# Optimization experiments

Hardware: AMD Instinct MI355X
Metric: run time of the kernel (lower is better)

The kernel has to match this reference:

```python
import jax, jax.numpy as jnp
import numpy as np

B, T, N, D, H = 16, 12, 325, 64, 4
E = 2600
NEG_SLOPE = 0.2
LN_EPS = 1e-5
SM_EPS = 1e-16


def setup_inputs() -> dict:
    key = jax.random.key(0)
    ks = jax.random.split(key, 8)
    x = jax.random.normal(ks[0], (B, T, N, D), dtype=jnp.float32)
    edge_index = jax.random.randint(ks[1], (2, E), 0, N, dtype=jnp.int64)
    W = jax.random.normal(ks[2], (D, H, D), dtype=jnp.float32) * 0.05   # lin weight, [in, heads, out]
    att_src = jax.random.normal(ks[3], (H, D), dtype=jnp.float32) * 0.05
    att_dst = jax.random.normal(ks[4], (H, D), dtype=jnp.float32) * 0.05
    bias = jnp.zeros((D,), dtype=jnp.float32)
    gamma = jnp.ones((D,), dtype=jnp.float32)
    beta = jnp.zeros((D,), dtype=jnp.float32)
    return {"x": x, "W": W, "att_src": att_src, "att_dst": att_dst,
            "bias": bias, "gamma": gamma, "beta": beta, "edge_index": edge_index}


def reference(x, W, att_src, att_dst, bias, gamma, beta, edge_index):
    b, t, n, d = x.shape
    bt = b * t
    xb = x.reshape(bt, n, d)

    # add self-loops (GATConv default add_self_loops=True)
    loops = jnp.arange(n, dtype=edge_index.dtype)
    src = jnp.concatenate([edge_index[0], loops])  # message source j
    dst = jnp.concatenate([edge_index[1], loops])  # message target i

    # per-head linear projection, node axis leading for segment ops: [N, BT, H, D]
    xp = jnp.einsum('bnd,dhf->nbhf', xb, W)

    a_src = jnp.einsum('nbhf,hf->nbh', xp, att_src)  # [N, BT, H]
    a_dst = jnp.einsum('nbhf,hf->nbh', xp, att_dst)

    alpha = a_src[src] + a_dst[dst]                  # [Etot, BT, H]
    alpha = jnp.where(alpha >= 0, alpha, NEG_SLOPE * alpha)

    # segment softmax over incoming edges of each dst node
    m = jax.ops.segment_max(alpha, dst, num_segments=n)        # [N, BT, H]
    e = jnp.exp(alpha - m[dst])
    s = jax.ops.segment_sum(e, dst, num_segments=n)            # [N, BT, H]
    coef = e / (s[dst] + SM_EPS)                               # [Etot, BT, H]

    # weighted scatter-sum aggregation
    msgs = coef[..., None] * xp[src]                           # [Etot, BT, H, D]
    out = jax.ops.segment_sum(msgs, dst, num_segments=n)       # [N, BT, H, D]

    out = out.mean(axis=2) + bias                              # concat=False -> head mean; [N, BT, D]
    out = out.transpose(1, 0, 2).reshape(b, t, n, d)

    # residual + LayerNorm
    y = x + out
    mu = y.mean(axis=-1, keepdims=True)
    var = y.var(axis=-1, keepdims=True)
    return (y - mu) * jax.lax.rsqrt(var + LN_EPS) * gamma + beta
```

## Files before the change

kernel.cpp:

```cpp
#include <hip/hip_runtime.h>

#define Nn 325
#define Dd 64
#define Hh 4
#define Ee 2600
#define BT 192
#define ETOT (Ee+Nn)
#define NROWS (BT*Nn)
#define XPS 136

#define XP_B   (Nn * XPS * 2)
#define COEF_B (ETOT * 8)
#define SMEM_BYTES (XP_B + COEF_B + 2600 + 2600 + ((Nn + 1) * 4) + (ETOT * 4) + (Nn * 4))

typedef __attribute__((ext_vector_type(8))) short bf16x8;
typedef __attribute__((ext_vector_type(4))) float f32x4;

static __device__ __forceinline__ short f2bf(float f) {
    union { float f; unsigned u; } v; v.f = f;
    unsigned r = v.u + 0x7fffu + ((v.u >> 16) & 1u);
    return (short)(r >> 16);
}
static __device__ __forceinline__ float bf_lo(unsigned p) {
    union { unsigned u; float f; } v; v.u = p << 16; return v.f;
}
static __device__ __forceinline__ float bf_hi(unsigned p) {
    union { unsigned u; float f; } v; v.u = p & 0xffff0000u; return v.f;
}

__global__ __launch_bounds__(256) void k_pre(
    const float* __restrict__ W, unsigned short* __restrict__ Wt,
    const int* __restrict__ ei, int* __restrict__ offs, int* __restrict__ elist,
    int* __restrict__ perm, const float* __restrict__ x,
    unsigned short* __restrict__ xbf)
{
    const int t = threadIdx.x;
    if (blockIdx.x < 64) {
        const int f = blockIdx.x * 256 + t;
        const int thr = f >> 6, idx = f & 63;
        const int ct = idx >> 4, kk = (idx >> 3) & 1, j = idx & 7;
        const int w = thr >> 6, lane = thr & 63;
        const int q = lane >> 4, l16 = lane & 15;
        Wt[f] = (unsigned short)f2bf(
            W[(size_t)(kk * 32 + q * 8 + j) * 256 + w * 64 + ct * 16 + l16]);
        return;
    }
    if (blockIdx.x >= 65) {
        const int bx = blockIdx.x - 65;
        #pragma unroll
        for (int k = 0; k < 8; ++k) {
            const int idx = bx * 2048 + k * 256 + t;
            if (idx < (NROWS * Dd) / 4) {
                float4 v = ((const float4*)x)[idx];
                ushort4 o;
                o.x = (unsigned short)f2bf(v.x);
                o.y = (unsigned short)f2bf(v.y);
                o.z = (unsigned short)f2bf(v.z);
                o.w = (unsigned short)f2bf(v.w);
                ((ushort4*)xbf)[idx] = o;
            }
        }
        return;
    }
    __shared__ int cnt[Nn + 1];
    __shared__ int cur[Nn];
    __shared__ int dh[64];
    __shared__ int startS[64];
    const int lane = t & 63;
    for (int i = t; i <= Nn; i += 256) cnt[i] = 0;
    if (t < 64) dh[t] = 0;
    __syncthreads();
    for (int e = t; e < ETOT; e += 256) {
        int d = (e < Ee) ? ei[Ee + e] : (e - Ee);
        atomicAdd(&cnt[d + 1], 1);
    }
    __syncthreads();
    if (t < 64) {
        int run = 0;
        for (int c = 0; c < 6; ++c) {
            int i = c * 64 + lane;
            int v = (i <= Nn) ? cnt[i] : 0;
            #pragma unroll
            for (int off = 1; off < 64; off <<= 1) {
                int u = __shfl_up(v, off);
                if (lane >= off) v += u;
            }
            v += run;
            if (i <= Nn) cnt[i] = v;
            run = __shfl(v, 63);
        }
    }
    __syncthreads();
    for (int i = t; i <= Nn; i += 256) offs[i] = cnt[i];
    for (int i = t; i < Nn; i += 256) cur[i] = cnt[i];
    for (int n = t; n < Nn; n += 256)
        atomicAdd(&dh[min(cnt[n + 1] - cnt[n], 63)], 1);
    __syncthreads();
    if (t < 64) {
        int v = dh[63 - lane];
        int inc = v;
        #pragma unroll
        for (int off = 1; off < 64; off <<= 1) {
            int u = __shfl_up(inc, off);
            if (lane >= off) inc += u;
        }
        startS[63 - lane] = inc - v;
    }
    __syncthreads();
    for (int e = t; e < ETOT; e += 256) {
        int s, d;
        if (e < Ee) { s = ei[e]; d = ei[Ee + e]; }
        else        { s = e - Ee; d = e - Ee; }
        int slot = atomicAdd(&cur[d], 1);
        elist[slot] = s;
    }
    for (int n = t; n < Nn; n += 256) {
        int slot = atomicAdd(&startS[min(cnt[n + 1] - cnt[n], 63)], 1);
        perm[slot] = n;
    }
}

__global__ __launch_bounds__(1024, 4) void k_fused(
    const float* __restrict__ x, const unsigned short* __restrict__ xbf,
    const unsigned short* __restrict__ Wt,
    const float* __restrict__ att_src, const float* __restrict__ att_dst,
    const int* __restrict__ offs, const int* __restrict__ elist,
    const int* __restrict__ perm,
    const float* __restrict__ bias, const float* __restrict__ gamma,
    const float* __restrict__ beta, float* __restrict__ out)
{
    const int bt   = blockIdx.x;
    const int t    = threadIdx.x;
    const int wv   = t >> 6;
    const int lane = t & 63;
    const int q    = lane >> 4;
    const int l16  = lane & 15;
    const int btN  = bt * Nn;

    extern __shared__ char smem[];
    unsigned short* xpS   = (unsigned short*)smem;
    float2*         coefS = (float2*)(smem + XP_B);
    float*          asrcS = (float*)(smem + XP_B + COEF_B);
    float*          adstS = asrcS + 2 * Nn;
    int*            offsS = (int*)(adstS + 2 * Nn);
    int*            elistS= offsS + (Nn + 1);
    int*            permS = elistS + ETOT;

    for (int i = t; i < ETOT; i += 1024) elistS[i] = elist[i];
    for (int i = t; i <= Nn; i += 1024) offsS[i] = offs[i];
    for (int i = t; i < Nn; i += 1024) permS[i] = perm[i];

    float accO[6][4];
    #pragma unroll
    for (int i = 0; i < 6; ++i)
        accO[i][0] = accO[i][1] = accO[i][2] = accO[i][3] = 0.f;

    const int hh  = wv >> 3;
    const int rtb = wv & 7;
    const int g   = wv * 4 + q;

    #pragma unroll 2
    for (int p = 0; p < 2; ++p) {
        const int h = p * 2 + hh;
        bf16x8 bfr[4][2];
        const bf16x8* wtp = (const bf16x8*)(Wt + (size_t)(h * 64 + lane) * 64);
        #pragma unroll
        for (int ct = 0; ct < 4; ++ct) {
            bfr[ct][0] = wtp[ct * 2];
            bfr[ct][1] = wtp[ct * 2 + 1];
        }
        float avs[4], avd[4];
        #pragma unroll
        for (int ct = 0; ct < 4; ++ct) {
            avs[ct] = att_src[h * 64 + ct * 16 + l16];
            avd[ct] = att_dst[h * 64 + ct * 16 + l16];
        }
        if (p) __syncthreads();

        #pragma unroll
        for (int k3 = 0; k3 < 3; ++k3) {
            const int rt = rtb + 8 * k3;
            if (rt > 20) break;
            const int na = min(rt * 16 + l16, Nn - 1);
            bf16x8 afr[2];
            #pragma unroll
            for (int kk = 0; kk < 2; ++kk)
                afr[kk] = *(const bf16x8*)(xbf + (size_t)(btN + na) * 64 + kk * 32 + q * 8);
            f32x4 acc[4];
            #pragma unroll
            for (int ct = 0; ct < 4; ++ct) {
                acc[ct] = (f32x4){0.f, 0.f, 0.f, 0.f};
                acc[ct] = __builtin_amdgcn_mfma_f32_16x16x32_bf16(afr[0], bfr[ct][0], acc[ct], 0, 0, 0);
                acc[ct] = __builtin_amdgcn_mfma_f32_16x16x32_bf16(afr[1], bfr[ct][1], acc[ct], 0, 0, 0);
            }
            #pragma unroll
            for (int r = 0; r < 4; ++r) {
                const int n = rt * 16 + q * 4 + r;
                float ps = 0.f, pd = 0.f;
                #pragma unroll
                for (int ct = 0; ct < 4; ++ct) {
                    ps = fmaf(acc[ct][r], avs[ct], ps);
                    pd = fmaf(acc[ct][r], avd[ct], pd);
                }
                #pragma unroll
                for (int off = 1; off <= 8; off <<= 1) {
                    ps += __shfl_xor(ps, off);
                    pd += __shfl_xor(pd, off);
                }
                if (l16 == 0 && n < Nn) {
                    asrcS[n * 2 + hh] = ps;
                    adstS[n * 2 + hh] = pd;
                }
                if (n < Nn) {
                    #pragma unroll
                    for (int ct = 0; ct < 4; ++ct)
                        xpS[n * XPS + (ct * 16 + l16) * 2 + hh] =
                            (unsigned short)f2bf(acc[ct][r]);
                }
            }
        }
        __syncthreads();

        #pragma unroll
        for (int it = 0; it < 6; ++it) {
            const int rk = it * 64 + g;
            if (rk >= Nn) continue;
            const int n = permS[rk];
            const int o0 = offsS[n];
            int deg = offsS[n + 1] - o0;
            deg = min(deg, 48);
            const float adn0 = adstS[n * 2], adn1 = adstS[n * 2 + 1];
            float ex0[3], ex1[3];
            float m0 = -3e38f, m1 = -3e38f;
            #pragma unroll
            for (int r = 0; r < 3; ++r) {
                float a0 = -3e38f, a1 = -3e38f;
                if (r * 16 < deg) {
                    const int e = r * 16 + l16;
                    if (e < deg) {
                        const int j = elistS[o0 + e];
                        const float2 as = *(const float2*)(asrcS + j * 2);
                        a0 = as.x + adn0; a1 = as.y + adn1;
                    }
                }
                a0 = (a0 >= 0.f) ? a0 : 0.2f * a0;
                a1 = (a1 >= 0.f) ? a1 : 0.2f * a1;
                ex0[r] = a0; ex1[r] = a1;
                m0 = fmaxf(m0, a0); m1 = fmaxf(m1, a1);
            }
            #pragma unroll
            for (int off = 1; off <= 8; off <<= 1) {
                m0 = fmaxf(m0, __shfl_xor(m0, off));
                m1 = fmaxf(m1, __shfl_xor(m1, off));
            }
            float s0 = 0.f, s1 = 0.f;
            #pragma unroll
            for (int r = 0; r < 3; ++r) if (r * 16 < deg) {
                ex0[r] = __expf(ex0[r] - m0); s0 += ex0[r];
                ex1[r] = __expf(ex1[r] - m1); s1 += ex1[r];
            }
            #pragma unroll
            for (int off = 1; off <= 8; off <<= 1) {
                s0 += __shfl_xor(s0, off);
                s1 += __shfl_xor(s1, off);
            }
            const float i0 = 1.f / (s0 + 1e-16f);
            const float i1 = 1.f / (s1 + 1e-16f);
            #pragma unroll
            for (int r = 0; r < 3; ++r) if (r * 16 < deg) {
                const int e = r * 16 + l16;
                if (e < deg) coefS[o0 + e] = make_float2(ex0[r] * i0, ex1[r] * i1);
            }

            float f0 = 0.f, f1 = 0.f, f2v = 0.f, f3 = 0.f;
            int e2 = 0;
            for (; e2 + 4 <= deg; e2 += 4) {
                const int j0 = elistS[o0 + e2],     j1 = elistS[o0 + e2 + 1];
                const int j2 = elistS[o0 + e2 + 2], j3 = elistS[o0 + e2 + 3];
                const float2 c0 = coefS[o0 + e2],     c1 = coefS[o0 + e2 + 1];
                const float2 c2 = coefS[o0 + e2 + 2], c3 = coefS[o0 + e2 + 3];
                const uint4 r0 = *(const uint4*)((const char*)xpS + j0 * (XPS * 2) + l16 * 16);
                const uint4 r1 = *(const uint4*)((const char*)xpS + j1 * (XPS * 2) + l16 * 16);
                const uint4 r2 = *(const uint4*)((const char*)xpS + j2 * (XPS * 2) + l16 * 16);
                const uint4 r3 = *(const uint4*)((const char*)xpS + j3 * (XPS * 2) + l16 * 16);
                f0  = fmaf(c0.x, bf_lo(r0.x), f0);  f0  = fmaf(c0.y, bf_hi(r0.x), f0);
                f1  = fmaf(c0.x, bf_lo(r0.y), f1);  f1  = fmaf(c0.y, bf_hi(r0.y), f1);
                f2v = fmaf(c0.x, bf_lo(r0.z), f2v); f2v = fmaf(c0.y, bf_hi(r0.z), f2v);
                f3  = fmaf(c0.x, bf_lo(r0.w), f3);  f3  = fmaf(c0.y, bf_hi(r0.w), f3);
                f0  = fmaf(c1.x, bf_lo(r1.x), f0);  f0  = fmaf(c1.y, bf_hi(r1.x), f0);
                f1  = fmaf(c1.x, bf_lo(r1.y), f1);  f1  = fmaf(c1.y, bf_hi(r1.y), f1);
                f2v = fmaf(c1.x, bf_lo(r1.z), f2v); f2v = fmaf(c1.y, bf_hi(r1.z), f2v);
                f3  = fmaf(c1.x, bf_lo(r1.w), f3);  f3  = fmaf(c1.y, bf_hi(r1.w), f3);
                f0  = fmaf(c2.x, bf_lo(r2.x), f0);  f0  = fmaf(c2.y, bf_hi(r2.x), f0);
                f1  = fmaf(c2.x, bf_lo(r2.y), f1);  f1  = fmaf(c2.y, bf_hi(r2.y), f1);
                f2v = fmaf(c2.x, bf_lo(r2.z), f2v); f2v = fmaf(c2.y, bf_hi(r2.z), f2v);
                f3  = fmaf(c2.x, bf_lo(r2.w), f3);  f3  = fmaf(c2.y, bf_hi(r2.w), f3);
                f0  = fmaf(c3.x, bf_lo(r3.x), f0);  f0  = fmaf(c3.y, bf_hi(r3.x), f0);
                f1  = fmaf(c3.x, bf_lo(r3.y), f1);  f1  = fmaf(c3.y, bf_hi(r3.y), f1);
                f2v = fmaf(c3.x, bf_lo(r3.z), f2v); f2v = fmaf(c3.y, bf_hi(r3.z), f2v);
                f3  = fmaf(c3.x, bf_lo(r3.w), f3);  f3  = fmaf(c3.y, bf_hi(r3.w), f3);
            }
            for (; e2 < deg; ++e2) {
                const int ja = elistS[o0 + e2];
                const float2 ca = coefS[o0 + e2];
                const uint4 ra = *(const uint4*)((const char*)xpS + ja * (XPS * 2) + l16 * 16);
                f0  = fmaf(ca.x, bf_lo(ra.x), f0);  f0  = fmaf(ca.y, bf_hi(ra.x), f0);
                f1  = fmaf(ca.x, bf_lo(ra.y), f1);  f1  = fmaf(ca.y, bf_hi(ra.y), f1);
                f2v = fmaf(ca.x, bf_lo(ra.z), f2v); f2v = fmaf(ca.y, bf_hi(ra.z), f2v);
                f3  = fmaf(ca.x, bf_lo(ra.w), f3);  f3  = fmaf(ca.y, bf_hi(ra.w), f3);
            }
            accO[it][0] += f0; accO[it][1] += f1;
            accO[it][2] += f2v; accO[it][3] += f3;
        }
    }

    const int f4 = l16 * 4;
    const float4 ga = *(const float4*)(gamma + f4);
    const float4 be = *(const float4*)(beta + f4);
    const float4 bi = *(const float4*)(bias + f4);
    #pragma unroll
    for (int it = 0; it < 6; ++it) {
        const int rk = it * 64 + g;
        if (rk >= Nn) continue;
        const int n = permS[rk];
        const float4 xv = *(const float4*)(x + (size_t)(btN + n) * 64 + f4);
        const float y0 = xv.x + accO[it][0] * 0.25f + bi.x;
        const float y1 = xv.y + accO[it][1] * 0.25f + bi.y;
        const float y2 = xv.z + accO[it][2] * 0.25f + bi.z;
        const float y3 = xv.w + accO[it][3] * 0.25f + bi.w;
        float s1 = y0 + y1 + y2 + y3;
        float s2 = y0*y0 + y1*y1 + y2*y2 + y3*y3;
        #pragma unroll
        for (int off = 1; off <= 8; off <<= 1) {
            s1 += __shfl_xor(s1, off);
            s2 += __shfl_xor(s2, off);
        }
        const float mu  = s1 * (1.f / 64.f);
        const float var = s2 * (1.f / 64.f) - mu * mu;
        const float rr  = rsqrtf(var + 1e-5f);
        float4 o;
        o.x = (y0 - mu) * rr * ga.x + be.x;
        o.y = (y1 - mu) * rr * ga.y + be.y;
        o.z = (y2 - mu) * rr * ga.z + be.z;
        o.w = (y3 - mu) * rr * ga.w + be.w;
        *(float4*)(out + (size_t)(btN + n) * 64 + f4) = o;
    }
}

extern "C" void kernel_launch(void* const* d_in, const int* in_sizes, int n_in,
                              void* d_out, int out_size, void* d_ws, size_t ws_size,
                              hipStream_t stream)
{
    const float* x       = (const float*)d_in[0];
    const float* W       = (const float*)d_in[1];
    const float* att_src = (const float*)d_in[2];
    const float* att_dst = (const float*)d_in[3];
    const float* bias    = (const float*)d_in[4];
    const float* gamma   = (const float*)d_in[5];
    const float* beta    = (const float*)d_in[6];
    const int*   ei      = (const int*)d_in[7];

    unsigned short* Wt  = (unsigned short*)d_ws;
    unsigned short* xbf = Wt + 16384;
    int* offs  = (int*)(xbf + (size_t)NROWS * Dd);
    int* elist = offs + (Nn + 1);
    int* perm  = elist + ETOT;
    float* out = (float*)d_out;

    hipFuncSetAttribute((const void*)k_fused,
                        hipFuncAttributeMaxDynamicSharedMemorySize, SMEM_BYTES);

    hipLaunchKernelGGL(k_pre, dim3(65 + 488), dim3(256), 0, stream,
                       W, Wt, ei, offs, elist, perm, x, xbf);
    hipLaunchKernelGGL(k_fused, dim3(BT), dim3(1024), SMEM_BYTES, stream,
                       x, xbf, Wt, att_src, att_dst, offs, elist, perm,
                       bias, gamma, beta, out);
}
```

Before: 134.4 us.

## Fold preprocessing kernel into fused GAT kernel and pipeline aggregation loads

Removes the separate preprocessing kernel. Each block now builds the CSR edge list and degree-sorted permutation in shared memory itself, converts W and x to bf16 on the fly from global fp32, and skips the bf16 copy of x in workspace. This avoids a kernel launch and a full write/read round trip of the x-sized bf16 buffer. In exchange every one of the 192 blocks repeats the CSR build and the W conversion with strided scalar loads. The aggregation loop also gains software prefetching of the next edge indices and coefficients, and uses packed float2 FMAs.

```diff
diff --git a/kernel.cpp b/kernel.cpp
--- a/kernel.cpp
+++ b/kernel.cpp
@@ -6,7 +6,6 @@
 #define Ee 2600
 #define BT 192
 #define ETOT (Ee+Nn)
-#define NROWS (BT*Nn)
 #define XPS 136
 
 #define XP_B   (Nn * XPS * 2)
@@ -15,117 +14,23 @@
 
 typedef __attribute__((ext_vector_type(8))) short bf16x8;
 typedef __attribute__((ext_vector_type(4))) float f32x4;
+typedef __attribute__((ext_vector_type(2))) float f32x2;
 
 static __device__ __forceinline__ short f2bf(float f) {
     union { float f; unsigned u; } v; v.f = f;
     unsigned r = v.u + 0x7fffu + ((v.u >> 16) & 1u);
     return (short)(r >> 16);
 }
-static __device__ __forceinline__ float bf_lo(unsigned p) {
-    union { unsigned u; float f; } v; v.u = p << 16; return v.f;
+static __device__ __forceinline__ f32x2 up2(unsigned u) {
+    union { unsigned u; float f; } lo, hi;
+    lo.u = u << 16; hi.u = u & 0xffff0000u;
+    f32x2 r; r.x = lo.f; r.y = hi.f; return r;
 }
-static __device__ __forceinline__ float bf_hi(unsigned p) {
-    union { unsigned u; float f; } v; v.u = p & 0xffff0000u; return v.f;
-}
-
-__global__ __launch_bounds__(256) void k_pre(
-    const float* __restrict__ W, unsigned short* __restrict__ Wt,
-    const int* __restrict__ ei, int* __restrict__ offs, int* __restrict__ elist,
-    int* __restrict__ perm, const float* __restrict__ x,
-    unsigned short* __restrict__ xbf)
-{
-    const int t = threadIdx.x;
-    if (blockIdx.x < 64) {
-        const int f = blockIdx.x * 256 + t;
-        const int thr = f >> 6, idx = f & 63;
-        const int ct = idx >> 4, kk = (idx >> 3) & 1, j = idx & 7;
-        const int w = thr >> 6, lane = thr & 63;
-        const int q = lane >> 4, l16 = lane & 15;
-        Wt[f] = (unsigned short)f2bf(
-            W[(size_t)(kk * 32 + q * 8 + j) * 256 + w * 64 + ct * 16 + l16]);
-        return;
-    }
-    if (blockIdx.x >= 65) {
-        const int bx = blockIdx.x - 65;
-        #pragma unroll
-        for (int k = 0; k < 8; ++k) {
-            const int idx = bx * 2048 + k * 256 + t;
-            if (idx < (NROWS * Dd) / 4) {
-                float4 v = ((const float4*)x)[idx];
-                ushort4 o;
-                o.x = (unsigned short)f2bf(v.x);
-                o.y = (unsigned short)f2bf(v.y);
-                o.z = (unsigned short)f2bf(v.z);
-                o.w = (unsigned short)f2bf(v.w);
-                ((ushort4*)xbf)[idx] = o;
-            }
-        }
-        return;
-    }
-    __shared__ int cnt[Nn + 1];
-    __shared__ int cur[Nn];
-    __shared__ int dh[64];
-    __shared__ int startS[64];
-    const int lane = t & 63;
-    for (int i = t; i <= Nn; i += 256) cnt[i] = 0;
-    if (t < 64) dh[t] = 0;
-    __syncthreads();
-    for (int e = t; e < ETOT; e += 256) {
-        int d = (e < Ee) ? ei[Ee + e] : (e - Ee);
-        atomicAdd(&cnt[d + 1], 1);
-    }
-    __syncthreads();
-    if (t < 64) {
-        int run = 0;
-        for (int c = 0; c < 6; ++c) {
-            int i = c * 64 + lane;
-            int v = (i <= Nn) ? cnt[i] : 0;
-            #pragma unroll
-            for (int off = 1; off < 64; off <<= 1) {
-                int u = __shfl_up(v, off);
-                if (lane >= off) v += u;
-            }
-            v += run;
-            if (i <= Nn) cnt[i] = v;
-            run = __shfl(v, 63);
-        }
-    }
-    __syncthreads();
-    for (int i = t; i <= Nn; i += 256) offs[i] = cnt[i];
-    for (int i = t; i < Nn; i += 256) cur[i] = cnt[i];
-    for (int n = t; n < Nn; n += 256)
-        atomicAdd(&dh[min(cnt[n + 1] - cnt[n], 63)], 1);
-    __syncthreads();
-    if (t < 64) {
-        int v = dh[63 - lane];
-        int inc = v;
-        #pragma unroll
-        for (int off = 1; off < 64; off <<= 1) {
-            int u = __shfl_up(inc, off);
-            if (lane >= off) inc += u;
-        }
-        startS[63 - lane] = inc - v;
-    }
-    __syncthreads();
-    for (int e = t; e < ETOT; e += 256) {
-        int s, d;
-        if (e < Ee) { s = ei[e]; d = ei[Ee + e]; }
-        else        { s = e - Ee; d = e - Ee; }
-        int slot = atomicAdd(&cur[d], 1);
-        elist[slot] = s;
-    }
-    for (int n = t; n < Nn; n += 256) {
-        int slot = atomicAdd(&startS[min(cnt[n + 1] - cnt[n], 63)], 1);
-        perm[slot] = n;
-    }
-}
-
-__global__ __launch_bounds__(1024, 4) void k_fused(
-    const float* __restrict__ x, const unsigned short* __restrict__ xbf,
-    const unsigned short* __restrict__ Wt,
+
+__global__ __launch_bounds__(1024, 4) void k_gat(
+    const float* __restrict__ x, const float* __restrict__ W,
     const float* __restrict__ att_src, const float* __restrict__ att_dst,
-    const int* __restrict__ offs, const int* __restrict__ elist,
-    const int* __restrict__ perm,
+    const int* __restrict__ ei,
     const float* __restrict__ bias, const float* __restrict__ gamma,
     const float* __restrict__ beta, float* __restrict__ out)
 {
@@ -139,21 +44,75 @@
 
     extern __shared__ char smem[];
     unsigned short* xpS   = (unsigned short*)smem;
-    float2*         coefS = (float2*)(smem + XP_B);
+    f32x2*          coefS = (f32x2*)(smem + XP_B);
     float*          asrcS = (float*)(smem + XP_B + COEF_B);
     float*          adstS = asrcS + 2 * Nn;
     int*            offsS = (int*)(adstS + 2 * Nn);
     int*            elistS= offsS + (Nn + 1);
     int*            permS = elistS + ETOT;
-
-    for (int i = t; i < ETOT; i += 1024) elistS[i] = elist[i];
-    for (int i = t; i <= Nn; i += 1024) offsS[i] = offs[i];
-    for (int i = t; i < Nn; i += 1024) permS[i] = perm[i];
-
-    float accO[6][4];
+    int* cnt = (int*)(smem + XP_B);
+    int* cur = cnt + (Nn + 1);
+    int* dh  = cur + Nn;
+    int* stS = dh + 64;
+
+    for (int i = t; i <= Nn; i += 1024) cnt[i] = 0;
+    if (t < 64) dh[t] = 0;
+    __syncthreads();
+    for (int e = t; e < ETOT; e += 1024) {
+        int d = (e < Ee) ? ei[Ee + e] : (e - Ee);
+        atomicAdd(&cnt[d + 1], 1);
+    }
+    __syncthreads();
+    if (t < 64) {
+        int run = 0;
+        for (int c = 0; c < 6; ++c) {
+            int i = c * 64 + lane;
+            int v = (i <= Nn) ? cnt[i] : 0;
+            #pragma unroll
+            for (int off = 1; off < 64; off <<= 1) {
+                int u = __shfl_up(v, off);
+                if (lane >= off) v += u;
+            }
+            v += run;
+            if (i <= Nn) cnt[i] = v;
+            run = __shfl(v, 63);
+        }
+    }
+    __syncthreads();
+    for (int i = t; i <= Nn; i += 1024) offsS[i] = cnt[i];
+    for (int i = t; i < Nn; i += 1024) cur[i] = cnt[i];
+    for (int n = t; n < Nn; n += 1024)
+        atomicAdd(&dh[min(cnt[n + 1] - cnt[n], 63)], 1);
+    __syncthreads();
+    if (t < 64) {
+        int v = dh[63 - lane];
+        int inc = v;
+        #pragma unroll
+        for (int off = 1; off < 64; off <<= 1) {
+            int u = __shfl_up(inc, off);
+            if (lane >= off) inc += u;
+        }
+        stS[63 - lane] = inc - v;
+    }
+    __syncthreads();
+    for (int e = t; e < ETOT; e += 1024) {
+        int s, d;
+        if (e < Ee) { s = ei[e]; d = ei[Ee + e]; }
+        else        { s = e - Ee; d = e - Ee; }
+        int slot = atomicAdd(&cur[d], 1);
+        elistS[slot] = s;
+    }
+    for (int n = t; n < Nn; n += 1024) {
+        int slot = atomicAdd(&stS[min(offsS[n + 1] - offsS[n], 63)], 1);
+        permS[slot] = n;
+    }
+    __syncthreads();
+
+    f32x2 accO[6][4];
     #pragma unroll
     for (int i = 0; i < 6; ++i)
-        accO[i][0] = accO[i][1] = accO[i][2] = accO[i][3] = 0.f;
+        #pragma unroll
+        for (int j = 0; j < 4; ++j) { accO[i][j].x = 0.f; accO[i][j].y = 0.f; }
 
     const int hh  = wv >> 3;
     const int rtb = wv & 7;
@@ -163,11 +122,16 @@
     for (int p = 0; p < 2; ++p) {
         const int h = p * 2 + hh;
         bf16x8 bfr[4][2];
-        const bf16x8* wtp = (const bf16x8*)(Wt + (size_t)(h * 64 + lane) * 64);
         #pragma unroll
         for (int ct = 0; ct < 4; ++ct) {
-            bfr[ct][0] = wtp[ct * 2];
-            bfr[ct][1] = wtp[ct * 2 + 1];
+            #pragma unroll
+            for (int kk = 0; kk < 2; ++kk) {
+                bf16x8 fr;
+                #pragma unroll
+                for (int j = 0; j < 8; ++j)
+                    fr[j] = f2bf(W[(size_t)(kk * 32 + q * 8 + j) * 256 + h * 64 + ct * 16 + l16]);
+                bfr[ct][kk] = fr;
+            }
         }
         float avs[4], avd[4];
         #pragma unroll
@@ -182,10 +146,17 @@
             const int rt = rtb + 8 * k3;
             if (rt > 20) break;
             const int na = min(rt * 16 + l16, Nn - 1);
+            const float* xr = x + (size_t)(btN + na) * 64;
             bf16x8 afr[2];
             #pragma unroll
-            for (int kk = 0; kk < 2; ++kk)
-                afr[kk] = *(const bf16x8*)(xbf + (size_t)(btN + na) * 64 + kk * 32 + q * 8);
+            for (int kk = 0; kk < 2; ++kk) {
+                const float4 xa = *(const float4*)(xr + kk * 32 + q * 8);
+                const float4 xb = *(const float4*)(xr + kk * 32 + q * 8 + 4);
+                bf16x8 fr;
+                fr[0] = f2bf(xa.x); fr[1] = f2bf(xa.y); fr[2] = f2bf(xa.z); fr[3] = f2bf(xa.w);
+                fr[4] = f2bf(xb.x); fr[5] = f2bf(xb.y); fr[6] = f2bf(xb.z); fr[7] = f2bf(xb.w);
+                afr[kk] = fr;
+            }
             f32x4 acc[4];
             #pragma unroll
             for (int ct = 0; ct < 4; ++ct) {
@@ -269,48 +240,53 @@
             #pragma unroll
             for (int r = 0; r < 3; ++r) if (r * 16 < deg) {
                 const int e = r * 16 + l16;
-                if (e < deg) coefS[o0 + e] = make_float2(ex0[r] * i0, ex1[r] * i1);
-            }
-
-            float f0 = 0.f, f1 = 0.f, f2v = 0.f, f3 = 0.f;
+                if (e < deg) {
+                    f32x2 cw; cw.x = ex0[r] * i0; cw.y = ex1[r] * i1;
+                    coefS[o0 + e] = cw;
+                }
+            }
+
+            f32x2 g0 = {0.f, 0.f}, g1 = {0.f, 0.f}, g2 = {0.f, 0.f}, g3 = {0.f, 0.f};
+#define MAC(c, r) do { \
+                g0 += (c) * up2((r).x); \
+                g1 += (c) * up2((r).y); \
+                g2 += (c) * up2((r).z); \
+                g3 += (c) * up2((r).w); \
+            } while (0)
             int e2 = 0;
-            for (; e2 + 4 <= deg; e2 += 4) {
-                const int j0 = elistS[o0 + e2],     j1 = elistS[o0 + e2 + 1];
-                const int j2 = elistS[o0 + e2 + 2], j3 = elistS[o0 + e2 + 3];
-                const float2 c0 = coefS[o0 + e2],     c1 = coefS[o0 + e2 + 1];
-                const float2 c2 = coefS[o0 + e2 + 2], c3 = coefS[o0 + e2 + 3];
-                const uint4 r0 = *(const uint4*)((const char*)xpS + j0 * (XPS * 2) + l16 * 16);
-                const uint4 r1 = *(const uint4*)((const char*)xpS + j1 * (XPS * 2) + l16 * 16);
-                const uint4 r2 = *(const uint4*)((const char*)xpS + j2 * (XPS * 2) + l16 * 16);
-                const uint4 r3 = *(const uint4*)((const char*)xpS + j3 * (XPS * 2) + l16 * 16);
-                f0  = fmaf(c0.x, bf_lo(r0.x), f0);  f0  = fmaf(c0.y, bf_hi(r0.x), f0);
-                f1  = fmaf(c0.x, bf_lo(r0.y), f1);  f1  = fmaf(c0.y, bf_hi(r0.y), f1);
-                f2v = fmaf(c0.x, bf_lo(r0.z), f2v); f2v = fmaf(c0.y, bf_hi(r0.z), f2v);
-                f3  = fmaf(c0.x, bf_lo(r0.w), f3);  f3  = fmaf(c0.y, bf_hi(r0.w), f3);
-                f0  = fmaf(c1.x, bf_lo(r1.x), f0);  f0  = fmaf(c1.y, bf_hi(r1.x), f0);
-                f1  = fmaf(c1.x, bf_lo(r1.y), f1);  f1  = fmaf(c1.y, bf_hi(r1.y), f1);
-                f2v = fmaf(c1.x, bf_lo(r1.z), f2v); f2v = fmaf(c1.y, bf_hi(r1.z), f2v);
-                f3  = fmaf(c1.x, bf_lo(r1.w), f3);  f3  = fmaf(c1.y, bf_hi(r1.w), f3);
-                f0  = fmaf(c2.x, bf_lo(r2.x), f0);  f0  = fmaf(c2.y, bf_hi(r2.x), f0);
-                f1  = fmaf(c2.x, bf_lo(r2.y), f1);  f1  = fmaf(c2.y, bf_hi(r2.y), f1);
-                f2v = fmaf(c2.x, bf_lo(r2.z), f2v); f2v = fmaf(c2.y, bf_hi(r2.z), f2v);
-                f3  = fmaf(c2.x, bf_lo(r2.w), f3);  f3  = fmaf(c2.y, bf_hi(r2.w), f3);
-                f0  = fmaf(c3.x, bf_lo(r3.x), f0);  f0  = fmaf(c3.y, bf_hi(r3.x), f0);
-                f1  = fmaf(c3.x, bf_lo(r3.y), f1);  f1  = fmaf(c3.y, bf_hi(r3.y), f1);
-                f2v = fmaf(c3.x, bf_lo(r3.z), f2v); f2v = fmaf(c3.y, bf_hi(r3.z), f2v);
-                f3  = fmaf(c3.x, bf_lo(r3.w), f3);  f3  = fmaf(c3.y, bf_hi(r3.w), f3);
+            if (deg >= 4) {
+                int j0 = elistS[o0 + 0], j1 = elistS[o0 + 1];
+                int j2 = elistS[o0 + 2], j3 = elistS[o0 + 3];
+                f32x2 c0 = coefS[o0 + 0], c1 = coefS[o0 + 1];
+                f32x2 c2 = coefS[o0 + 2], c3 = coefS[o0 + 3];
+                while (true) {
+                    const char* bp = (const char*)xpS + l16 * 16;
+                    const uint4 r0 = *(const uint4*)(bp + j0 * (XPS * 2));
+                    const uint4 r1 = *(const uint4*)(bp + j1 * (XPS * 2));
+                    const uint4 r2 = *(const uint4*)(bp + j2 * (XPS * 2));
+                    const uint4 r3 = *(const uint4*)(bp + j3 * (XPS * 2));
+                    e2 += 4;
+                    const bool more = (e2 + 4 <= deg);
+                    const int nb = o0 + (more ? e2 : (deg - 4));
+                    const int nj0 = elistS[nb + 0], nj1 = elistS[nb + 1];
+                    const int nj2 = elistS[nb + 2], nj3 = elistS[nb + 3];
+                    const f32x2 nc0 = coefS[nb + 0], nc1 = coefS[nb + 1];
+                    const f32x2 nc2 = coefS[nb + 2], nc3 = coefS[nb + 3];
+                    MAC(c0, r0); MAC(c1, r1); MAC(c2, r2); MAC(c3, r3);
+                    j0 = nj0; j1 = nj1; j2 = nj2; j3 = nj3;
+                    c0 = nc0; c1 = nc1; c2 = nc2; c3 = nc3;
+                    if (!more) break;
+                }
             }
             for (; e2 < deg; ++e2) {
                 const int ja = elistS[o0 + e2];
-                const float2 ca = coefS[o0 + e2];
+                const f32x2 ca = coefS[o0 + e2];
                 const uint4 ra = *(const uint4*)((const char*)xpS + ja * (XPS * 2) + l16 * 16);
-                f0  = fmaf(ca.x, bf_lo(ra.x), f0);  f0  = fmaf(ca.y, bf_hi(ra.x), f0);
-                f1  = fmaf(ca.x, bf_lo(ra.y), f1);  f1  = fmaf(ca.y, bf_hi(ra.y), f1);
-                f2v = fmaf(ca.x, bf_lo(ra.z), f2v); f2v = fmaf(ca.y, bf_hi(ra.z), f2v);
-                f3  = fmaf(ca.x, bf_lo(ra.w), f3);  f3  = fmaf(ca.y, bf_hi(ra.w), f3);
-            }
-            accO[it][0] += f0; accO[it][1] += f1;
-            accO[it][2] += f2v; accO[it][3] += f3;
+                MAC(ca, ra);
+            }
+#undef MAC
+            accO[it][0] += g0; accO[it][1] += g1;
+            accO[it][2] += g2; accO[it][3] += g3;
         }
     }
 
@@ -324,10 +300,10 @@
         if (rk >= Nn) continue;
         const int n = permS[rk];
         const float4 xv = *(const float4*)(x + (size_t)(btN + n) * 64 + f4);
-        const float y0 = xv.x + accO[it][0] * 0.25f + bi.x;
-        const float y1 = xv.y + accO[it][1] * 0.25f + bi.y;
-        const float y2 = xv.z + accO[it][2] * 0.25f + bi.z;
-        const float y3 = xv.w + accO[it][3] * 0.25f + bi.w;
+        const float y0 = xv.x + (accO[it][0].x + accO[it][0].y) * 0.25f + bi.x;
+        const float y1 = xv.y + (accO[it][1].x + accO[it][1].y) * 0.25f + bi.y;
+        const float y2 = xv.z + (accO[it][2].x + accO[it][2].y) * 0.25f + bi.z;
+        const float y3 = xv.w + (accO[it][3].x + accO[it][3].y) * 0.25f + bi.w;
         float s1 = y0 + y1 + y2 + y3;
         float s2 = y0*y0 + y1*y1 + y2*y2 + y3*y3;
         #pragma unroll
@@ -359,20 +335,12 @@
     const float* gamma   = (const float*)d_in[5];
     const float* beta    = (const float*)d_in[6];
     const int*   ei      = (const int*)d_in[7];
-
-    unsigned short* Wt  = (unsigned short*)d_ws;
-    unsigned short* xbf = Wt + 16384;
-    int* offs  = (int*)(xbf + (size_t)NROWS * Dd);
-    int* elist = offs + (Nn + 1);
-    int* perm  = elist + ETOT;
     float* out = (float*)d_out;
-
-    hipFuncSetAttribute((const void*)k_fused,
+    (void)in_sizes; (void)n_in; (void)out_size; (void)d_ws; (void)ws_size;
+
+    hipFuncSetAttribute((const void*)k_gat,
                         hipFuncAttributeMaxDynamicSharedMemorySize, SMEM_BYTES);
 
-    hipLaunchKernelGGL(k_pre, dim3(65 + 488), dim3(256), 0, stream,
-                       W, Wt, ei, offs, elist, perm, x, xbf);
-    hipLaunchKernelGGL(k_fused, dim3(BT), dim3(1024), SMEM_BYTES, stream,
-                       x, xbf, Wt, att_src, att_dst, offs, elist, perm,
-                       bias, gamma, beta, out);
+    hipLaunchKernelGGL(k_gat, dim3(BT), dim3(1024), SMEM_BYTES, stream,
+                       x, W, att_src, att_dst, ei, bias, gamma, beta, out);
 }
```

Result: slower. 140.6 us (+4.7%).

## Software-pipeline edge gather loop and use packed float2 FMAs for aggregation

Applied to the files above, without the earlier changes.

Restructures the per-node aggregation loop so the LDS loads of xp rows, coefficients and edge indices for the next group of four edges are issued before the current group's FMAs, hiding LDS latency. The accumulation is rewritten as paired float2 multiply-adds so the compiler can emit packed FP32 FMA instructions, with the two head halves summed at the end. The score-computation phase also hoists the edge-index and a_src loads ahead of the arithmetic. This adds register pressure and changes the order of floating-point summation.

```diff
diff --git a/kernel.cpp b/kernel.cpp
--- a/kernel.cpp
+++ b/kernel.cpp
@@ -15,17 +15,17 @@
 
 typedef __attribute__((ext_vector_type(8))) short bf16x8;
 typedef __attribute__((ext_vector_type(4))) float f32x4;
+typedef __attribute__((ext_vector_type(2))) float f32x2;
 
 static __device__ __forceinline__ short f2bf(float f) {
     union { float f; unsigned u; } v; v.f = f;
     unsigned r = v.u + 0x7fffu + ((v.u >> 16) & 1u);
     return (short)(r >> 16);
 }
-static __device__ __forceinline__ float bf_lo(unsigned p) {
-    union { unsigned u; float f; } v; v.u = p << 16; return v.f;
-}
-static __device__ __forceinline__ float bf_hi(unsigned p) {
-    union { unsigned u; float f; } v; v.u = p & 0xffff0000u; return v.f;
+static __device__ __forceinline__ f32x2 up2(unsigned u) {
+    union { unsigned u; float f; } lo, hi;
+    lo.u = u << 16; hi.u = u & 0xffff0000u;
+    f32x2 r; r.x = lo.f; r.y = hi.f; return r;
 }
 
 __global__ __launch_bounds__(256) void k_pre(
@@ -158,6 +158,7 @@
     const int hh  = wv >> 3;
     const int rtb = wv & 7;
     const int g   = wv * 4 + q;
+    const char* bp = (const char*)xpS + l16 * 16;
 
     #pragma unroll 2
     for (int p = 0; p < 2; ++p) {
@@ -230,18 +231,24 @@
             int deg = offsS[n + 1] - o0;
             deg = min(deg, 48);
             const float adn0 = adstS[n * 2], adn1 = adstS[n * 2 + 1];
+
+            const int nch = (deg + 15) >> 4;
+            int jv[3]; float2 asr[3];
+            #pragma unroll
+            for (int r = 0; r < 3; ++r)
+                if (r < nch) jv[r] = elistS[o0 + min(r * 16 + l16, deg - 1)];
+            #pragma unroll
+            for (int r = 0; r < 3; ++r)
+                if (r < nch) asr[r] = *(const float2*)(asrcS + jv[r] * 2);
+
             float ex0[3], ex1[3];
             float m0 = -3e38f, m1 = -3e38f;
             #pragma unroll
             for (int r = 0; r < 3; ++r) {
                 float a0 = -3e38f, a1 = -3e38f;
-                if (r * 16 < deg) {
+                if (r < nch) {
                     const int e = r * 16 + l16;
-                    if (e < deg) {
-                        const int j = elistS[o0 + e];
-                        const float2 as = *(const float2*)(asrcS + j * 2);
-                        a0 = as.x + adn0; a1 = as.y + adn1;
-                    }
+                    if (e < deg) { a0 = asr[r].x + adn0; a1 = asr[r].y + adn1; }
                 }
                 a0 = (a0 >= 0.f) ? a0 : 0.2f * a0;
                 a1 = (a1 >= 0.f) ? a1 : 0.2f * a1;
@@ -255,7 +262,7 @@
             }
             float s0 = 0.f, s1 = 0.f;
             #pragma unroll
-            for (int r = 0; r < 3; ++r) if (r * 16 < deg) {
+            for (int r = 0; r < 3; ++r) if (r < nch) {
                 ex0[r] = __expf(ex0[r] - m0); s0 += ex0[r];
                 ex1[r] = __expf(ex1[r] - m1); s1 += ex1[r];
             }
@@ -267,50 +274,63 @@
             const float i0 = 1.f / (s0 + 1e-16f);
             const float i1 = 1.f / (s1 + 1e-16f);
             #pragma unroll
-            for (int r = 0; r < 3; ++r) if (r * 16 < deg) {
+            for (int r = 0; r < 3; ++r) if (r < nch) {
                 const int e = r * 16 + l16;
                 if (e < deg) coefS[o0 + e] = make_float2(ex0[r] * i0, ex1[r] * i1);
             }
 
-            float f0 = 0.f, f1 = 0.f, f2v = 0.f, f3 = 0.f;
+            f32x2 g0 = {0.f, 0.f}, g1 = {0.f, 0.f}, g2 = {0.f, 0.f}, g3 = {0.f, 0.f};
+#define MACQ(c, r) do { \
+                const f32x2 cc = {(c).x, (c).y}; \
+                g0 += cc * up2((r).x); \
+                g1 += cc * up2((r).y); \
+                g2 += cc * up2((r).z); \
+                g3 += cc * up2((r).w); \
+            } while (0)
             int e2 = 0;
-            for (; e2 + 4 <= deg; e2 += 4) {
-                const int j0 = elistS[o0 + e2],     j1 = elistS[o0 + e2 + 1];
-                const int j2 = elistS[o0 + e2 + 2], j3 = elistS[o0 + e2 + 3];
-                const float2 c0 = coefS[o0 + e2],     c1 = coefS[o0 + e2 + 1];
-                const float2 c2 = coefS[o0 + e2 + 2], c3 = coefS[o0 + e2 + 3];
-                const uint4 r0 = *(const uint4*)((const char*)xpS + j0 * (XPS * 2) + l16 * 16);
-                const uint4 r1 = *(const uint4*)((const char*)xpS + j1 * (XPS * 2) + l16 * 16);
-                const uint4 r2 = *(const uint4*)((const char*)xpS + j2 * (XPS * 2) + l16 * 16);
-                const uint4 r3 = *(const uint4*)((const char*)xpS + j3 * (XPS * 2) + l16 * 16);
-                f0  = fmaf(c0.x, bf_lo(r0.x), f0);  f0  = fmaf(c0.y, bf_hi(r0.x), f0);
-                f1  = fmaf(c0.x, bf_lo(r0.y), f1);  f1  = fmaf(c0.y, bf_hi(r0.y), f1);
-                f2v = fmaf(c0.x, bf_lo(r0.z), f2v); f2v = fmaf(c0.y, bf_hi(r0.z), f2v);
-                f3  = fmaf(c0.x, bf_lo(r0.w), f3);  f3  = fmaf(c0.y, bf_hi(r0.w), f3);
-                f0  = fmaf(c1.x, bf_lo(r1.x), f0);  f0  = fmaf(c1.y, bf_hi(r1.x), f0);
-                f1  = fmaf(c1.x, bf_lo(r1.y), f1);  f1  = fmaf(c1.y, bf_hi(r1.y), f1);
-                f2v = fmaf(c1.x, bf_lo(r1.z), f2v); f2v = fmaf(c1.y, bf_hi(r1.z), f2v);
-                f3  = fmaf(c1.x, bf_lo(r1.w), f3);  f3  = fmaf(c1.y, bf_hi(r1.w), f3);
-                f0  = fmaf(c2.x, bf_lo(r2.x), f0);  f0  = fmaf(c2.y, bf_hi(r2.x), f0);
-                f1  = fmaf(c2.x, bf_lo(r2.y), f1);  f1  = fmaf(c2.y, bf_hi(r2.y), f1);
-                f2v = fmaf(c2.x, bf_lo(r2.z), f2v); f2v = fmaf(c2.y, bf_hi(r2.z), f2v);
-                f3  = fmaf(c2.x, bf_lo(r2.w), f3);  f3  = fmaf(c2.y, bf_hi(r2.w), f3);
-                f0  = fmaf(c3.x, bf_lo(r3.x), f0);  f0  = fmaf(c3.y, bf_hi(r3.x), f0);
-                f1  = fmaf(c3.x, bf_lo(r3.y), f1);  f1  = fmaf(c3.y, bf_hi(r3.y), f1);
-                f2v = fmaf(c3.x, bf_lo(r3.z), f2v); f2v = fmaf(c3.y, bf_hi(r3.z), f2v);
-                f3  = fmaf(c3.x, bf_lo(r3.w), f3);  f3  = fmaf(c3.y, bf_hi(r3.w), f3);
+            if (deg >= 4) {
+                const int jA0 = elistS[o0 + 0], jA1 = elistS[o0 + 1];
+                const int jA2 = elistS[o0 + 2], jA3 = elistS[o0 + 3];
+                float2 cA0 = coefS[o0 + 0], cA1 = coefS[o0 + 1];
+                float2 cA2 = coefS[o0 + 2], cA3 = coefS[o0 + 3];
+                uint4 rA0 = *(const uint4*)(bp + jA0 * (XPS * 2));
+                uint4 rA1 = *(const uint4*)(bp + jA1 * (XPS * 2));
+                uint4 rA2 = *(const uint4*)(bp + jA2 * (XPS * 2));
+                uint4 rA3 = *(const uint4*)(bp + jA3 * (XPS * 2));
+                const int nb1 = o0 + ((deg >= 8) ? 4 : 0);
+                int jB0 = elistS[nb1 + 0], jB1 = elistS[nb1 + 1];
+                int jB2 = elistS[nb1 + 2], jB3 = elistS[nb1 + 3];
+                while (true) {
+                    const bool moreB = (e2 + 8 <= deg);
+                    const uint4 rB0 = *(const uint4*)(bp + jB0 * (XPS * 2));
+                    const uint4 rB1 = *(const uint4*)(bp + jB1 * (XPS * 2));
+                    const uint4 rB2 = *(const uint4*)(bp + jB2 * (XPS * 2));
+                    const uint4 rB3 = *(const uint4*)(bp + jB3 * (XPS * 2));
+                    const int nbB = o0 + min(e2 + 4, deg - 4);
+                    const float2 cB0 = coefS[nbB + 0], cB1 = coefS[nbB + 1];
+                    const float2 cB2 = coefS[nbB + 2], cB3 = coefS[nbB + 3];
+                    const int nbC = o0 + min(e2 + 8, deg - 4);
+                    const int jC0 = elistS[nbC + 0], jC1 = elistS[nbC + 1];
+                    const int jC2 = elistS[nbC + 2], jC3 = elistS[nbC + 3];
+                    MACQ(cA0, rA0); MACQ(cA1, rA1); MACQ(cA2, rA2); MACQ(cA3, rA3);
+                    e2 += 4;
+                    if (!moreB) break;
+                    rA0 = rB0; rA1 = rB1; rA2 = rB2; rA3 = rB3;
+                    cA0 = cB0; cA1 = cB1; cA2 = cB2; cA3 = cB3;
+                    jB0 = jC0; jB1 = jC1; jB2 = jC2; jB3 = jC3;
+                }
             }
             for (; e2 < deg; ++e2) {
                 const int ja = elistS[o0 + e2];
                 const float2 ca = coefS[o0 + e2];
-                const uint4 ra = *(const uint4*)((const char*)xpS + ja * (XPS * 2) + l16 * 16);
-                f0  = fmaf(ca.x, bf_lo(ra.x), f0);  f0  = fmaf(ca.y, bf_hi(ra.x), f0);
-                f1  = fmaf(ca.x, bf_lo(ra.y), f1);  f1  = fmaf(ca.y, bf_hi(ra.y), f1);
-                f2v = fmaf(ca.x, bf_lo(ra.z), f2v); f2v = fmaf(ca.y, bf_hi(ra.z), f2v);
-                f3  = fmaf(ca.x, bf_lo(ra.w), f3);  f3  = fmaf(ca.y, bf_hi(ra.w), f3);
-            }
-            accO[it][0] += f0; accO[it][1] += f1;
-            accO[it][2] += f2v; accO[it][3] += f3;
+                const uint4 ra = *(const uint4*)(bp + ja * (XPS * 2));
+                MACQ(ca, ra);
+            }
+#undef MACQ
+            accO[it][0] += g0.x + g0.y;
+            accO[it][1] += g1.x + g1.y;
+            accO[it][2] += g2.x + g2.y;
+            accO[it][3] += g3.x + g3.y;
         }
     }
 
```

New measurement: 139.1 us. 1.04x slower.

## Split fused GAT kernel into projection and per-node gather kernels via global workspace

Applied to the files above, without the earlier changes.

Replaces the single per-bt fused kernel (192 blocks of 1024 threads) with a projection kernel that writes bf16 projected features and attention logits to global memory, followed by a gather kernel that spreads the softmax, aggregation and LayerNorm across 1536 smaller blocks at wavefront-per-node granularity. The preprocessing kernel no longer converts x to bf16; the projection reads fp32 x directly. The aim is better occupancy and load balance in the gather phase, at the cost of an extra launch and a global round-trip of the projected features (about 32 MB). Node degree is capped at 48 in the gather kernel, which could silently drop edges for high-degree nodes. The old path remains as a fallback when the workspace is too small.

```diff
diff --git a/kernel.cpp b/kernel.cpp
--- a/kernel.cpp
+++ b/kernel.cpp
@@ -6,10 +6,11 @@
 #define Ee 2600
 #define BT 192
 #define ETOT (Ee+Nn)
-#define NROWS (BT*Nn)
+#define TOTAL (BT*Nn)
+#define NROWS TOTAL
 #define XPS 136
-
-#define XP_B   (Nn * XPS * 2)
+#define XP_B (Nn * XPS * 2)
+
 #define COEF_B (ETOT * 8)
 #define SMEM_BYTES (XP_B + COEF_B + 2600 + 2600 + ((Nn + 1) * 4) + (ETOT * 4) + (Nn * 4))
 
@@ -28,7 +29,284 @@
     union { unsigned u; float f; } v; v.u = p & 0xffff0000u; return v.f;
 }
 
-__global__ __launch_bounds__(256) void k_pre(
+
+__global__ __launch_bounds__(256) void k_pre_s(
+    const float* __restrict__ W, unsigned short* __restrict__ Wt,
+    const int* __restrict__ ei, int* __restrict__ offs, int* __restrict__ elist)
+{
+    const int t = threadIdx.x;
+    if (blockIdx.x < 64) {
+        const int f = blockIdx.x * 256 + t;
+        const int thr = f >> 6, idx = f & 63;
+        const int ct = idx >> 4, kk = (idx >> 3) & 1, j = idx & 7;
+        const int w = thr >> 6, lane = thr & 63;
+        const int q = lane >> 4, l16 = lane & 15;
+        Wt[f] = (unsigned short)f2bf(
+            W[(size_t)(kk * 32 + q * 8 + j) * 256 + w * 64 + ct * 16 + l16]);
+        return;
+    }
+    __shared__ int cnt[Nn + 1];
+    __shared__ int cur[Nn];
+    const int lane = t & 63;
+    for (int i = t; i <= Nn; i += 256) cnt[i] = 0;
+    __syncthreads();
+    for (int e = t; e < ETOT; e += 256) {
+        int d = (e < Ee) ? ei[Ee + e] : (e - Ee);
+        atomicAdd(&cnt[d + 1], 1);
+    }
+    __syncthreads();
+    if (t < 64) {
+        int run = 0;
+        for (int c = 0; c < 6; ++c) {
+            int i = c * 64 + lane;
+            int v = (i <= Nn) ? cnt[i] : 0;
+            #pragma unroll
+            for (int off = 1; off < 64; off <<= 1) {
+                int u = __shfl_up(v, off);
+                if (lane >= off) v += u;
+            }
+            v += run;
+            if (i <= Nn) cnt[i] = v;
+            run = __shfl(v, 63);
+        }
+    }
+    __syncthreads();
+    for (int i = t; i <= Nn; i += 256) offs[i] = cnt[i];
+    for (int i = t; i < Nn; i += 256) cur[i] = cnt[i];
+    __syncthreads();
+    for (int e = t; e < ETOT; e += 256) {
+        int s, d;
+        if (e < Ee) { s = ei[e]; d = ei[Ee + e]; }
+        else        { s = e - Ee; d = e - Ee; }
+        int slot = atomicAdd(&cur[d], 1);
+        elist[slot] = s;
+    }
+}
+
+__global__ __launch_bounds__(1024, 4) void k_proj(
+    const float* __restrict__ x, const unsigned short* __restrict__ Wt,
+    const float* __restrict__ att_src, const float* __restrict__ att_dst,
+    unsigned short* __restrict__ xpG, float* __restrict__ asrcG,
+    float* __restrict__ adstG)
+{
+    const int bt   = blockIdx.x;
+    const int t    = threadIdx.x;
+    const int wv   = t >> 6;
+    const int lane = t & 63;
+    const int q    = lane >> 4;
+    const int l16  = lane & 15;
+    const int btN  = bt * Nn;
+
+    extern __shared__ char smem[];
+    unsigned short* xpS = (unsigned short*)smem;
+
+    const int hh  = wv >> 3;
+    const int rtb = wv & 7;
+
+    #pragma unroll 2
+    for (int p = 0; p < 2; ++p) {
+        const int h = p * 2 + hh;
+        bf16x8 bfr[4][2];
+        const bf16x8* wtp = (const bf16x8*)(Wt + (size_t)(h * 64 + lane) * 64);
+        #pragma unroll
+        for (int ct = 0; ct < 4; ++ct) {
+            bfr[ct][0] = wtp[ct * 2];
+            bfr[ct][1] = wtp[ct * 2 + 1];
+        }
+        float avs[4], avd[4];
+        #pragma unroll
+        for (int ct = 0; ct < 4; ++ct) {
+            avs[ct] = att_src[h * 64 + ct * 16 + l16];
+            avd[ct] = att_dst[h * 64 + ct * 16 + l16];
+        }
+        if (p) __syncthreads();
+
+        #pragma unroll
+        for (int k3 = 0; k3 < 3; ++k3) {
+            const int rt = rtb + 8 * k3;
+            if (rt > 20) break;
+            const int na = min(rt * 16 + l16, Nn - 1);
+            const float* xr = x + (size_t)(btN + na) * 64;
+            bf16x8 afr[2];
+            #pragma unroll
+            for (int kk = 0; kk < 2; ++kk) {
+                const float4 xa = *(const float4*)(xr + kk * 32 + q * 8);
+                const float4 xb = *(const float4*)(xr + kk * 32 + q * 8 + 4);
+                bf16x8 fr;
+                fr[0] = f2bf(xa.x); fr[1] = f2bf(xa.y); fr[2] = f2bf(xa.z); fr[3] = f2bf(xa.w);
+                fr[4] = f2bf(xb.x); fr[5] = f2bf(xb.y); fr[6] = f2bf(xb.z); fr[7] = f2bf(xb.w);
+                afr[kk] = fr;
+            }
+            f32x4 acc[4];
+            #pragma unroll
+            for (int ct = 0; ct < 4; ++ct) {
+                acc[ct] = (f32x4){0.f, 0.f, 0.f, 0.f};
+                acc[ct] = __builtin_amdgcn_mfma_f32_16x16x32_bf16(afr[0], bfr[ct][0], acc[ct], 0, 0, 0);
+                acc[ct] = __builtin_amdgcn_mfma_f32_16x16x32_bf16(afr[1], bfr[ct][1], acc[ct], 0, 0, 0);
+            }
+            #pragma unroll
+            for (int r = 0; r < 4; ++r) {
+                const int n = rt * 16 + q * 4 + r;
+                float ps = 0.f, pd = 0.f;
+                #pragma unroll
+                for (int ct = 0; ct < 4; ++ct) {
+                    ps = fmaf(acc[ct][r], avs[ct], ps);
+                    pd = fmaf(acc[ct][r], avd[ct], pd);
+                }
+                #pragma unroll
+                for (int off = 1; off <= 8; off <<= 1) {
+                    ps += __shfl_xor(ps, off);
+                    pd += __shfl_xor(pd, off);
+                }
+                if (l16 == 0 && n < Nn) {
+                    asrcG[(btN + n) * 4 + h] = ps;
+                    adstG[(btN + n) * 4 + h] = pd;
+                }
+                if (n < Nn) {
+                    #pragma unroll
+                    for (int ct = 0; ct < 4; ++ct)
+                        xpS[n * XPS + (ct * 16 + l16) * 2 + hh] =
+                            (unsigned short)f2bf(acc[ct][r]);
+                }
+            }
+        }
+        __syncthreads();
+        const uint4* src = (const uint4*)xpS;
+        uint4*       dst = (uint4*)xpG;
+        for (int i = t; i < Nn * 16; i += 1024) {
+            const int row = i >> 4, c16 = i & 15;
+            dst[(size_t)(btN + row) * 32 + p * 16 + c16] = src[row * 17 + c16];
+        }
+    }
+}
+
+#define GBLK 1536
+#define WPT  11
+__global__ __launch_bounds__(256, 4) void k_gather(
+    const unsigned short* __restrict__ xpG, const float* __restrict__ asrcG,
+    const float* __restrict__ adstG, const int* __restrict__ offs,
+    const int* __restrict__ elist, const float* __restrict__ x,
+    const float* __restrict__ bias, const float* __restrict__ gamma,
+    const float* __restrict__ beta, float* __restrict__ out)
+{
+    __shared__ float coefL[4][48][4];
+    __shared__ int   jLs[4][48];
+    const int wv   = threadIdx.x >> 6;
+    const int lane = threadIdx.x & 63;
+    const int l16  = lane & 15;
+    const int h    = lane >> 4;
+    const int half = lane >> 5;
+    const int d0   = (lane & 31) * 2;
+    const unsigned laneoff = (unsigned)(half * 256 + (lane & 31) * 8);
+
+    const int bsw = (blockIdx.x & 7) * 192 + (blockIdx.x >> 3);
+    const int gw  = bsw * 4 + wv;
+    const int u0  = gw * WPT;
+    const int uE  = min(u0 + WPT, TOTAL);
+
+    const float2 bi = *(const float2*)(bias + d0);
+    const float2 ga = *(const float2*)(gamma + d0);
+    const float2 be = *(const float2*)(beta + d0);
+
+    for (int u = u0; u < uE; ++u) {
+        const int bt  = u / Nn;
+        const int n   = u - bt * Nn;
+        const int btN = bt * Nn;
+
+        const int o0 = offs[n];
+        int deg = offs[n + 1] - o0;
+        deg = min(deg, 48);
+        const int nch = (deg + 15) >> 4;
+        const float adv = adstG[(btN + n) * 4 + h];
+        float ex[3]; int jreg[3];
+        float m = -3e38f;
+        #pragma unroll
+        for (int r = 0; r < 3; ++r) {
+            float a = -3e38f;
+            if (r < nch) {
+                const int e = r * 16 + l16;
+                const int j = elist[o0 + min(e, deg - 1)];
+                jreg[r] = j;
+                if (e < deg) {
+                    const float av = asrcG[(btN + j) * 4 + h];
+                    a = av + adv;
+                    a = (a >= 0.f) ? a : 0.2f * a;
+                }
+            }
+            ex[r] = a;
+            m = fmaxf(m, a);
+        }
+        #pragma unroll
+        for (int off = 1; off <= 8; off <<= 1)
+            m = fmaxf(m, __shfl_xor(m, off));
+        float s = 0.f;
+        #pragma unroll
+        for (int r = 0; r < 3; ++r) if (r < nch) {
+            ex[r] = __expf(ex[r] - m);
+            s += ex[r];
+        }
+        #pragma unroll
+        for (int off = 1; off <= 8; off <<= 1)
+            s += __shfl_xor(s, off);
+        const float inv = 1.f / (s + 1e-16f);
+        #pragma unroll
+        for (int r = 0; r < 3; ++r) if (r < nch) {
+            const int e = r * 16 + l16;
+            if (e < deg) {
+                coefL[wv][e][h] = ex[r] * inv;
+                if (h == 0) jLs[wv][e] = jreg[r];
+            }
+        }
+
+        float a00 = 0.f, a01 = 0.f, a10 = 0.f, a11 = 0.f;
+        for (int eb = 0; eb < deg; eb += 8) {
+            const int ne = min(deg - eb, 8);
+            int jv[8];
+            #pragma unroll
+            for (int k = 0; k < 8; ++k) if (k < ne) jv[k] = jLs[wv][eb + k];
+            float2 cc[8]; uint2 rr[8];
+            #pragma unroll
+            for (int k = 0; k < 8; ++k) if (k < ne) {
+                cc[k] = *(const float2*)(&coefL[wv][eb + k][half * 2]);
+                const unsigned off = ((unsigned)(btN + jv[k]) << 9) + laneoff;
+                rr[k] = *(const uint2*)((const char*)xpG + off);
+            }
+            #pragma unroll
+            for (int k = 0; k < 8; ++k) if (k < ne) {
+                a00 = fmaf(cc[k].x, bf_lo(rr[k].x), a00);
+                a01 = fmaf(cc[k].y, bf_hi(rr[k].x), a01);
+                a10 = fmaf(cc[k].x, bf_lo(rr[k].y), a10);
+                a11 = fmaf(cc[k].y, bf_hi(rr[k].y), a11);
+            }
+        }
+
+        float t0 = a00 + a01, t1 = a10 + a11;
+        t0 += __shfl_xor(t0, 32);
+        t1 += __shfl_xor(t1, 32);
+        const float2 xv = *(const float2*)(x + (size_t)u * 64 + d0);
+        const float y0 = xv.x + t0 * 0.25f + bi.x;
+        const float y1 = xv.y + t1 * 0.25f + bi.y;
+        float s1 = y0 + y1;
+        float s2 = y0 * y0 + y1 * y1;
+        #pragma unroll
+        for (int off = 1; off <= 16; off <<= 1) {
+            s1 += __shfl_xor(s1, off);
+            s2 += __shfl_xor(s2, off);
+        }
+        const float mu  = s1 * (1.f / 64.f);
+        const float var = s2 * (1.f / 64.f) - mu * mu;
+        const float rs  = rsqrtf(var + 1e-5f);
+        if (lane < 32) {
+            float2 o;
+            o.x = (y0 - mu) * rs * ga.x + be.x;
+            o.y = (y1 - mu) * rs * ga.y + be.y;
+            *(float2*)(out + (size_t)u * 64 + d0) = o;
+        }
+    }
+}
+
+
+__global__ __launch_bounds__(256) void k_pre_f(
     const float* __restrict__ W, unsigned short* __restrict__ Wt,
     const int* __restrict__ ei, int* __restrict__ offs, int* __restrict__ elist,
     int* __restrict__ perm, const float* __restrict__ x,
@@ -347,6 +625,7 @@
     }
 }
 
+
 extern "C" void kernel_launch(void* const* d_in, const int* in_sizes, int n_in,
                               void* d_out, int out_size, void* d_ws, size_t ws_size,
                               hipStream_t stream)
@@ -359,20 +638,45 @@
     const float* gamma   = (const float*)d_in[5];
     const float* beta    = (const float*)d_in[6];
     const int*   ei      = (const int*)d_in[7];
-
-    unsigned short* Wt  = (unsigned short*)d_ws;
-    unsigned short* xbf = Wt + 16384;
-    int* offs  = (int*)(xbf + (size_t)NROWS * Dd);
-    int* elist = offs + (Nn + 1);
-    int* perm  = elist + ETOT;
     float* out = (float*)d_out;
-
-    hipFuncSetAttribute((const void*)k_fused,
-                        hipFuncAttributeMaxDynamicSharedMemorySize, SMEM_BYTES);
-
-    hipLaunchKernelGGL(k_pre, dim3(65 + 488), dim3(256), 0, stream,
-                       W, Wt, ei, offs, elist, perm, x, xbf);
-    hipLaunchKernelGGL(k_fused, dim3(BT), dim3(1024), SMEM_BYTES, stream,
-                       x, xbf, Wt, att_src, att_dst, offs, elist, perm,
-                       bias, gamma, beta, out);
-}
+    (void)in_sizes; (void)n_in; (void)out_size;
+
+    const size_t hdr    = (32768 + (326 + 2925) * 4 + 15) & ~(size_t)15;
+    const size_t asz    = (size_t)TOTAL * 4 * 4;
+    const size_t xpsz   = (size_t)TOTAL * 256 * 2;
+    const size_t need   = hdr + 2 * asz + xpsz;
+
+    if (ws_size >= need) {
+        unsigned short* Wt    = (unsigned short*)d_ws;
+        int*            offs  = (int*)(Wt + 16384);
+        int*            elist = offs + 326;
+        char*           base  = (char*)d_ws + hdr;
+        float*          asrcG = (float*)base;
+        float*          adstG = asrcG + (size_t)TOTAL * 4;
+        unsigned short* xpG   = (unsigned short*)(adstG + (size_t)TOTAL * 4);
+
+        hipFuncSetAttribute((const void*)k_proj,
+                            hipFuncAttributeMaxDynamicSharedMemorySize, XP_B);
+
+        hipLaunchKernelGGL(k_pre_s, dim3(65), dim3(256), 0, stream, W, Wt, ei, offs, elist);
+        hipLaunchKernelGGL(k_proj, dim3(BT), dim3(1024), XP_B, stream,
+                           x, Wt, att_src, att_dst, xpG, asrcG, adstG);
+        hipLaunchKernelGGL(k_gather, dim3(GBLK), dim3(256), 0, stream,
+                           xpG, asrcG, adstG, offs, elist, x, bias, gamma, beta, out);
+    } else {
+        unsigned short* Wt  = (unsigned short*)d_ws;
+        unsigned short* xbf = Wt + 16384;
+        int* offs  = (int*)(xbf + (size_t)NROWS * Dd);
+        int* elist = offs + (Nn + 1);
+        int* perm  = elist + ETOT;
+
+        hipFuncSetAttribute((const void*)k_fused,
+                            hipFuncAttributeMaxDynamicSharedMemorySize, SMEM_BYTES);
+
+        hipLaunchKernelGGL(k_pre_f, dim3(65 + 488), dim3(256), 0, stream,
+                           W, Wt, ei, offs, elist, perm, x, xbf);
+        hipLaunchKernelGGL(k_fused, dim3(BT), dim3(1024), SMEM_BYTES, stream,
+                           x, xbf, Wt, att_src, att_dst, offs, elist, perm,
+                           bias, gamma, beta, out);
+    }
+}
```

After: 186.2 us. 38.6% more time.
